# Performance work log

Measured on AMD Instinct MI355X. Metric: run time of the kernel, lower is better.

The kernel has to match this reference:

```python
import jax, jax.numpy as jnp
import numpy as np

E, H, I = 8, 2048, 768  # num_experts, hidden_size, moe_intermediate_size
B, S = 4, 1024


def setup_inputs() -> dict:
    key = jax.random.key(0)
    k1, k2, k3, k4, k5 = jax.random.split(key, 5)
    hidden_states = jax.random.normal(k1, (B, S, H), dtype=jnp.float32)
    routing_weights = jax.random.uniform(k2, (B * S, E), dtype=jnp.float32)
    router_indices = jax.random.randint(k3, (B * S, 2), 0, E)
    gate_up_proj = jax.random.normal(k4, (E, H, 2 * I), dtype=jnp.float32) * 0.02
    down_proj = jax.random.normal(k5, (E, I, H), dtype=jnp.float32) * 0.02
    return {
        "hidden_states": hidden_states,
        "routing_weights": routing_weights,
        "router_indices": router_indices,
        "gate_up_proj": gate_up_proj,
        "down_proj": down_proj,
    }


def reference(hidden_states, routing_weights, router_indices, gate_up_proj, down_proj):
    b, s, h = hidden_states.shape
    x = hidden_states.reshape(-1, h)  # [T, H], T = B*S
    # dense all-experts: every token through every expert
    gate_up = jnp.einsum("th,ehd->etd", x, gate_up_proj)  # [E, T, 2I]
    gate, up = jnp.split(gate_up, 2, axis=-1)
    inter = up * jax.nn.silu(gate)  # [E, T, I]
    out = jnp.einsum("eti,eih->eth", inter, down_proj)  # [E, T, H]
    rw = routing_weights.T.reshape(out.shape[0], b, s)  # [E, B, S]
    out = out.reshape(out.shape[0], b, s, h) * rw[..., None]
    return out.sum(axis=0)  # [B, S, H]
```

## Files before the change

### kernel.cpp

```cpp
#include <hip/hip_runtime.h>
#include <cstdint>
#include <cstddef>

#define NE 8
#define NH 2048
#define NI 768
#define NT 4096
#define NK2 6144

typedef __bf16 bf16x8 __attribute__((ext_vector_type(8)));
typedef float f32x4 __attribute__((ext_vector_type(4)));
typedef unsigned short u16x8 __attribute__((ext_vector_type(8)));

__device__ __forceinline__ unsigned short f2bf(float f) {
  unsigned int u = __builtin_bit_cast(unsigned int, f);
  u += 0x7fffu + ((u >> 16) & 1u);
  return (unsigned short)(u >> 16);
}

__device__ __forceinline__ void gload_lds16(const void* g, void* s) {
  __builtin_amdgcn_global_load_lds(
      (const __attribute__((address_space(1))) unsigned int*)g,
      (__attribute__((address_space(3))) unsigned int*)s, 16, 0, 0);
}

__global__ __launch_bounds__(256) void k_cvt(const float* __restrict__ in,
                                             unsigned short* __restrict__ out,
                                             long n) {
  long i = ((long)blockIdx.x * blockDim.x + threadIdx.x) * 8;
  if (i >= n) return;
  float4 f0 = *reinterpret_cast<const float4*>(in + i);
  float4 f1 = *reinterpret_cast<const float4*>(in + i + 4);
  u16x8 o;
  o[0] = f2bf(f0.x); o[1] = f2bf(f0.y); o[2] = f2bf(f0.z); o[3] = f2bf(f0.w);
  o[4] = f2bf(f1.x); o[5] = f2bf(f1.y); o[6] = f2bf(f1.z); o[7] = f2bf(f1.w);
  *reinterpret_cast<u16x8*>(out + i) = o;
}

__global__ __launch_bounds__(256) void k_transpose_cvt(
    const float* __restrict__ in, unsigned short* __restrict__ out,
    int R, int C, long inBS, long outBS, int outCS, int mode) {
  __shared__ float tile[32][33];
  const int b = blockIdx.z;
  const int r0 = blockIdx.y * 32, c0 = blockIdx.x * 32;
  const int tx = threadIdx.x, ty = threadIdx.y;
  const float* ib = in + (long)b * inBS;
#pragma unroll
  for (int d = 0; d < 4; d++)
    tile[ty + d * 8][tx] = ib[(long)(r0 + ty + d * 8) * C + c0 + tx];
  __syncthreads();
#pragma unroll
  for (int d = 0; d < 4; d++) {
    int c = c0 + ty + d * 8;
    int r = r0 + tx;
    int orow;
    if (mode == 1) {
      int z = (c >= NI) ? 1 : 0;
      int cc = c - z * NI;
      orow = ((cc >> 4) << 5) + (z << 4) + (cc & 15);
    } else {
      orow = c;
    }
    out[(long)b * outBS + (long)orow * outCS + r] = f2bf(tile[tx][ty + d * 8]);
  }
}


__global__ __launch_bounds__(512, 2) void k_gemm1(
    const unsigned short* __restrict__ Xb,
    const unsigned short* __restrict__ W1t,
    const float* __restrict__ rw,
    unsigned short* __restrict__ inter) {
  __shared__ unsigned short lds[2][2][16384];

  const int e = blockIdx.z;
  const int t0 = blockIdx.y * 256;
  const int bn = blockIdx.x;
  const int tid = threadIdx.x;
  const int lane = tid & 63;
  const int wave = tid >> 6;
  const int wr = wave >> 2, wc = wave & 3;
  const int fr = lane & 15, fq = lane >> 4;

  const unsigned short* Ag = Xb;
  const unsigned short* Bg = W1t + (size_t)e * (2 * NI) * NH;
  const int rowA0 = t0, rowB0 = bn * 256;
  const int nkt = NH / 64;
  const int NIT = nkt / 2;

  const int cl0 = tid, cl1 = 512 + tid;
  const int rih0 = cl0 >> 3, ck0 = cl0 & 7;
  const int rih1 = cl1 >> 3, ck1 = cl1 & 7;
  const unsigned short* sA0q0 = Ag + (size_t)(rowA0 + rih0) * NH + ((ck0 ^ (rih0 & 7)) << 3);
  const unsigned short* sA0q1 = Ag + (size_t)(rowA0 + rih1) * NH + ((ck1 ^ (rih1 & 7)) << 3);
  const unsigned short* sA1q0 = Ag + (size_t)(rowA0 + 128 + rih0) * NH + ((ck0 ^ (rih0 & 7)) << 3);
  const unsigned short* sA1q1 = Ag + (size_t)(rowA0 + 128 + rih1) * NH + ((ck1 ^ (rih1 & 7)) << 3);
  const unsigned short* sB0q0 = Bg + (size_t)(rowB0 + rih0) * NH + ((ck0 ^ (rih0 & 7)) << 3);
  const unsigned short* sB0q1 = Bg + (size_t)(rowB0 + rih1) * NH + ((ck1 ^ (rih1 & 7)) << 3);
  const unsigned short* sB1q0 = Bg + (size_t)(rowB0 + 128 + rih0) * NH + ((ck0 ^ (rih0 & 7)) << 3);
  const unsigned short* sB1q1 = Bg + (size_t)(rowB0 + 128 + rih1) * NH + ((ck1 ^ (rih1 & 7)) << 3);
  const int d0 = cl0 * 8, d1 = cl1 * 8;

#define STG_A(BUFI, H, KT) do { \
    gload_lds16(sA##H##q0 + (size_t)(KT) * 64, &lds[BUFI][0][(H) * 8192 + d0]); \
    gload_lds16(sA##H##q1 + (size_t)(KT) * 64, &lds[BUFI][0][(H) * 8192 + d1]); \
  } while (0)
#define STG_B(BUFI, H, KT) do { \
    gload_lds16(sB##H##q0 + (size_t)(KT) * 64, &lds[BUFI][1][(H) * 8192 + d0]); \
    gload_lds16(sB##H##q1 + (size_t)(KT) * 64, &lds[BUFI][1][(H) * 8192 + d1]); \
  } while (0)

  f32x4 acc[8][4];
#pragma unroll
  for (int i = 0; i < 8; ++i)
#pragma unroll
    for (int j = 0; j < 4; ++j) acc[i][j] = (f32x4){0.f, 0.f, 0.f, 0.f};

  const int swz = fr & 7;

#define PHASE(BUFI, IH, JH, ISSUE, DOWAIT) do { \
    bf16x8 af[4][2], bf[2][2]; \
    _Pragma("unroll") \
    for (int ii = 0; ii < 4; ++ii) { \
      const int rA = (IH) * 128 + wr * 64 + ii * 16 + fr; \
      _Pragma("unroll") \
      for (int kk = 0; kk < 2; ++kk) \
        af[ii][kk] = *reinterpret_cast<const bf16x8*>( \
            &lds[BUFI][0][rA * 64 + (((kk * 4 + fq) ^ swz) << 3)]); \
    } \
    _Pragma("unroll") \
    for (int jj = 0; jj < 2; ++jj) { \
      const int rB = (JH) * 128 + wc * 32 + jj * 16 + fr; \
      _Pragma("unroll") \
      for (int kk = 0; kk < 2; ++kk) \
        bf[jj][kk] = *reinterpret_cast<const bf16x8*>( \
            &lds[BUFI][1][rB * 64 + (((kk * 4 + fq) ^ swz) << 3)]); \
    } \
    ISSUE; \
    if (DOWAIT) asm volatile("s_waitcnt vmcnt(4)" ::: "memory"); \
    __builtin_amdgcn_sched_barrier(0); \
    __builtin_amdgcn_s_barrier(); \
    __builtin_amdgcn_sched_barrier(0); \
    __builtin_amdgcn_s_setprio(1); \
    _Pragma("unroll") \
    for (int kk = 0; kk < 2; ++kk) \
      _Pragma("unroll") \
      for (int ii = 0; ii < 4; ++ii) \
        _Pragma("unroll") \
        for (int jj = 0; jj < 2; ++jj) \
          acc[(IH) * 4 + ii][(JH) * 2 + jj] = __builtin_amdgcn_mfma_f32_16x16x32_bf16( \
              af[ii][kk], bf[jj][kk], acc[(IH) * 4 + ii][(JH) * 2 + jj], 0, 0, 0); \
    __builtin_amdgcn_s_setprio(0); \
    __builtin_amdgcn_sched_barrier(0); \
    __builtin_amdgcn_s_barrier(); \
    __builtin_amdgcn_sched_barrier(0); \
  } while (0)

  STG_B(0, 0, 0); STG_A(0, 0, 0); STG_A(0, 1, 0); STG_B(0, 1, 0);
  STG_B(1, 0, 1); STG_A(1, 0, 1);
  asm volatile("s_waitcnt vmcnt(4)" ::: "memory");
  __builtin_amdgcn_sched_barrier(0);
  __builtin_amdgcn_s_barrier();
  __builtin_amdgcn_sched_barrier(0);

  for (int it = 0; it < NIT; ++it) {
    const int kt1 = 2 * it + 1;
    const int p0 = (2 * it + 2 < nkt) ? 2 * it + 2 : nkt - 1;
    const int p1 = (2 * it + 3 < nkt) ? 2 * it + 3 : nkt - 1;
    PHASE(0, 0, 0, STG_A(1, 1, kt1), 0);
    PHASE(0, 1, 0, STG_B(1, 1, kt1), 0);
    PHASE(0, 0, 1, STG_B(0, 0, p0), 0);
    PHASE(0, 1, 1, STG_A(0, 0, p0), 1);
    PHASE(1, 0, 0, STG_A(0, 1, p0), 0);
    PHASE(1, 1, 0, STG_B(0, 1, p0), 0);
    PHASE(1, 0, 1, STG_B(1, 0, p1), 0);
    PHASE(1, 1, 1, STG_A(1, 0, p1), 1);
  }
  asm volatile("s_waitcnt vmcnt(0)" ::: "memory");

#undef PHASE
#undef STG_A
#undef STG_B

#pragma unroll
  for (int i = 0; i < 8; ++i) {
    const int trow = t0 + (i >> 2) * 128 + wr * 64 + (i & 3) * 16 + fq * 4;
#pragma unroll
    for (int r = 0; r < 4; ++r) {
      const int t = trow + r;
      const float rwv = rw[(size_t)t * NE + e];
#pragma unroll
      for (int p = 0; p < 2; ++p) {
        float g = acc[i][2 * p][r];
        float u = acc[i][2 * p + 1][r];
        float s = g / (1.f + __expf(-g));
        const int col = bn * 128 + (p * 4 + wc) * 16 + fr;
        inter[(size_t)t * NK2 + e * NI + col] = f2bf(rwv * u * s);
      }
    }
  }
}

#define BUF_US 24576
#define B_OFF 16384

__device__ __forceinline__ void gemm_core(
    const unsigned short* __restrict__ A, int ldA, int rowA0,
    const unsigned short* __restrict__ B, int ldB, int rowB0,
    int nkt, unsigned short* lds, f32x4 acc[4][4]) {
  const int tid = threadIdx.x;
  const int lane = tid & 63;
  const int wave = tid >> 6;
  const int wr = wave >> 1;
  const int wc = wave & 1;
  const int fr = lane & 15, fq = lane >> 4;

  size_t sA[4]; int dA[4];
#pragma unroll
  for (int q = 0; q < 4; ++q) {
    int chunk = q * 512 + tid;
    int row = chunk >> 3, c = chunk & 7;
    sA[q] = (size_t)(rowA0 + row) * ldA + ((c ^ (row & 7)) << 3);
    dA[q] = chunk * 8;
  }
  size_t sB[2]; int dB[2];
#pragma unroll
  for (int q = 0; q < 2; ++q) {
    int chunk = q * 512 + tid;
    int row = chunk >> 3, c = chunk & 7;
    sB[q] = (size_t)(rowB0 + row) * ldB + ((c ^ (row & 7)) << 3);
    dB[q] = B_OFF + chunk * 8;
  }

  int aO[2][4], bO[2][4];
#pragma unroll
  for (int kk = 0; kk < 2; ++kk) {
#pragma unroll
    for (int i = 0; i < 4; ++i) {
      int rowA = wr * 64 + i * 16 + fr;
      aO[kk][i] = rowA * 64 + (((kk * 4 + fq) ^ (rowA & 7)) << 3);
      int rowB = wc * 64 + i * 16 + fr;
      bO[kk][i] = B_OFF + rowB * 64 + (((kk * 4 + fq) ^ (rowB & 7)) << 3);
    }
  }

#pragma unroll
  for (int i = 0; i < 4; ++i)
#pragma unroll
    for (int j = 0; j < 4; ++j) acc[i][j] = (f32x4){0.f, 0.f, 0.f, 0.f};

#pragma unroll
  for (int q = 0; q < 4; ++q) gload_lds16(A + sA[q], lds + dA[q]);
#pragma unroll
  for (int q = 0; q < 2; ++q) gload_lds16(B + sB[q], lds + dB[q]);
#pragma unroll
  for (int q = 0; q < 4; ++q) gload_lds16(A + sA[q] + 64, lds + BUF_US + dA[q]);
#pragma unroll
  for (int q = 0; q < 2; ++q) gload_lds16(B + sB[q] + 64, lds + BUF_US + dB[q]);

  int bi = 0, bs = 2;
  for (int kt = 0; kt < nkt; ++kt) {
    if (kt == nkt - 1) {
      asm volatile("s_waitcnt vmcnt(0)" ::: "memory");
    } else {
      asm volatile("s_waitcnt vmcnt(6)" ::: "memory");
    }
    __builtin_amdgcn_s_barrier();
    __builtin_amdgcn_sched_barrier(0);

    if (kt + 2 < nkt) {
      const int k0 = (kt + 2) * 64;
      unsigned short* tb = lds + bs * BUF_US;
#pragma unroll
      for (int q = 0; q < 4; ++q) gload_lds16(A + sA[q] + k0, tb + dA[q]);
#pragma unroll
      for (int q = 0; q < 2; ++q) gload_lds16(B + sB[q] + k0, tb + dB[q]);
    }

    const unsigned short* cb = lds + bi * BUF_US;
#pragma unroll
    for (int kk = 0; kk < 2; ++kk) {
      bf16x8 a[4], b[4];
#pragma unroll
      for (int i = 0; i < 4; ++i) a[i] = *reinterpret_cast<const bf16x8*>(cb + aO[kk][i]);
#pragma unroll
      for (int j = 0; j < 4; ++j) b[j] = *reinterpret_cast<const bf16x8*>(cb + bO[kk][j]);
      __builtin_amdgcn_s_setprio(1);
#pragma unroll
      for (int i = 0; i < 4; ++i)
#pragma unroll
        for (int j = 0; j < 4; ++j)
          acc[i][j] = __builtin_amdgcn_mfma_f32_16x16x32_bf16(a[i], b[j], acc[i][j], 0, 0, 0);
      __builtin_amdgcn_s_setprio(0);
    }

    bi = (bi == 2) ? 0 : bi + 1;
    bs = (bs == 2) ? 0 : bs + 1;
  }
}

__global__ __launch_bounds__(512, 2) void k_gemm2(
    const unsigned short* __restrict__ inter,
    const unsigned short* __restrict__ W2t,
    float* __restrict__ out) {
  __shared__ unsigned short lds[3 * BUF_US];
  const int t0 = blockIdx.y * 256;
  const int h0 = blockIdx.x * 128;
  f32x4 acc[4][4];
  gemm_core(inter, NK2, t0, W2t, NK2, h0, NK2 / 64, lds, acc);

  const int tid = threadIdx.x, lane = tid & 63, wave = tid >> 6;
  const int wr = wave >> 1, wc = wave & 1, fr = lane & 15, fq = lane >> 4;
  const int rowBase = t0 + wr * 64 + fq * 4;
#pragma unroll
  for (int i = 0; i < 4; ++i)
#pragma unroll
    for (int j = 0; j < 4; ++j)
#pragma unroll
      for (int r = 0; r < 4; ++r)
        out[(size_t)(rowBase + i * 16 + r) * NH + h0 + wc * 64 + j * 16 + fr] =
            acc[i][j][r];
}

extern "C" void kernel_launch(void* const* d_in, const int* in_sizes, int n_in,
                              void* d_out, int out_size, void* d_ws, size_t ws_size,
                              hipStream_t stream) {
  const float* x = (const float*)d_in[0];
  const float* rw = (const float*)d_in[1];
  const float* w1 = (const float*)d_in[3];
  const float* w2 = (const float*)d_in[4];
  float* out = (float*)d_out;

  char* ws = (char*)d_ws;
  unsigned short* Xb = (unsigned short*)ws;
  unsigned short* W1t = (unsigned short*)(ws + 16777216);
  unsigned short* W2t = (unsigned short*)(ws + 16777216 + 50331648);
  unsigned short* inter = (unsigned short*)(ws + 16777216 + 50331648 + 25165824);

  k_cvt<<<dim3((NT * NH) / (256 * 8)), dim3(256), 0, stream>>>(x, Xb, (long)NT * NH);
  k_transpose_cvt<<<dim3((2 * NI) / 32, NH / 32, NE), dim3(32, 8), 0, stream>>>(
      w1, W1t, NH, 2 * NI, (long)NH * 2 * NI, (long)2 * NI * NH, NH, 1);
  k_transpose_cvt<<<dim3(NH / 32, NI / 32, NE), dim3(32, 8), 0, stream>>>(
      w2, W2t, NI, NH, (long)NI * NH, (long)NI, NK2, 0);
  k_gemm1<<<dim3((2 * NI) / 256, NT / 256, NE), dim3(512), 0, stream>>>(Xb, W1t, rw, inter);
  k_gemm2<<<dim3(NH / 128, NT / 256), dim3(512), 0, stream>>>(inter, W2t, out);
}
```

Measured before the change: 372.2 us.

## Reuse B fragments across paired phases and drop trailing per-phase barrier

B-operand fragments are now loaded from LDS only on alternate phases and kept in registers for the next phase, which halves B LDS reads. The second workgroup barrier at the end of each phase is removed, leaving one barrier per phase. The order of the global-to-LDS staging calls is rearranged so that each buffer region is refilled only after every wave has passed the barrier following its last read. This cuts synchronization and LDS traffic, but it raises register pressure and depends on the new issue order being correct to avoid read/write races.

```diff
diff --git a/kernel.cpp b/kernel.cpp
--- a/kernel.cpp
+++ b/kernel.cpp
@@ -117,9 +117,20 @@
     for (int j = 0; j < 4; ++j) acc[i][j] = (f32x4){0.f, 0.f, 0.f, 0.f};
 
   const int swz = fr & 7;
-
-#define PHASE(BUFI, IH, JH, ISSUE, DOWAIT) do { \
-    bf16x8 af[4][2], bf[2][2]; \
+  bf16x8 bfr[2][2];
+
+#define PHASE(BUFI, IH, JH, RDB, ISSUE, DOWAIT) do { \
+    if (RDB) { \
+      _Pragma("unroll") \
+      for (int jj = 0; jj < 2; ++jj) { \
+        const int rB = (JH) * 128 + wc * 32 + jj * 16 + fr; \
+        _Pragma("unroll") \
+        for (int kk = 0; kk < 2; ++kk) \
+          bfr[jj][kk] = *reinterpret_cast<const bf16x8*>( \
+              &lds[BUFI][1][rB * 64 + (((kk * 4 + fq) ^ swz) << 3)]); \
+      } \
+    } \
+    bf16x8 af[4][2]; \
     _Pragma("unroll") \
     for (int ii = 0; ii < 4; ++ii) { \
       const int rA = (IH) * 128 + wr * 64 + ii * 16 + fr; \
@@ -127,14 +138,6 @@
       for (int kk = 0; kk < 2; ++kk) \
         af[ii][kk] = *reinterpret_cast<const bf16x8*>( \
             &lds[BUFI][0][rA * 64 + (((kk * 4 + fq) ^ swz) << 3)]); \
-    } \
-    _Pragma("unroll") \
-    for (int jj = 0; jj < 2; ++jj) { \
-      const int rB = (JH) * 128 + wc * 32 + jj * 16 + fr; \
-      _Pragma("unroll") \
-      for (int kk = 0; kk < 2; ++kk) \
-        bf[jj][kk] = *reinterpret_cast<const bf16x8*>( \
-            &lds[BUFI][1][rB * 64 + (((kk * 4 + fq) ^ swz) << 3)]); \
     } \
     ISSUE; \
     if (DOWAIT) asm volatile("s_waitcnt vmcnt(4)" ::: "memory"); \
@@ -149,10 +152,8 @@
         _Pragma("unroll") \
         for (int jj = 0; jj < 2; ++jj) \
           acc[(IH) * 4 + ii][(JH) * 2 + jj] = __builtin_amdgcn_mfma_f32_16x16x32_bf16( \
-              af[ii][kk], bf[jj][kk], acc[(IH) * 4 + ii][(JH) * 2 + jj], 0, 0, 0); \
+              af[ii][kk], bfr[jj][kk], acc[(IH) * 4 + ii][(JH) * 2 + jj], 0, 0, 0); \
     __builtin_amdgcn_s_setprio(0); \
-    __builtin_amdgcn_sched_barrier(0); \
-    __builtin_amdgcn_s_barrier(); \
     __builtin_amdgcn_sched_barrier(0); \
   } while (0)
 
@@ -165,16 +166,16 @@
 
   for (int it = 0; it < NIT; ++it) {
     const int kt1 = 2 * it + 1;
-    const int p0 = (2 * it + 2 < nkt) ? 2 * it + 2 : nkt - 1;
-    const int p1 = (2 * it + 3 < nkt) ? 2 * it + 3 : nkt - 1;
-    PHASE(0, 0, 0, STG_A(1, 1, kt1), 0);
-    PHASE(0, 1, 0, STG_B(1, 1, kt1), 0);
-    PHASE(0, 0, 1, STG_B(0, 0, p0), 0);
-    PHASE(0, 1, 1, STG_A(0, 0, p0), 1);
-    PHASE(1, 0, 0, STG_A(0, 1, p0), 0);
-    PHASE(1, 1, 0, STG_B(0, 1, p0), 0);
-    PHASE(1, 0, 1, STG_B(1, 0, p1), 0);
-    PHASE(1, 1, 1, STG_A(1, 0, p1), 1);
+    const int kt2 = (2 * it + 2 < nkt) ? 2 * it + 2 : nkt - 1;
+    const int kt3 = (2 * it + 3 < nkt) ? 2 * it + 3 : nkt - 1;
+    PHASE(0, 0, 0, 1, STG_B(1, 1, kt1), 0);
+    PHASE(0, 1, 0, 0, STG_A(1, 1, kt1), 0);
+    PHASE(0, 0, 1, 1, STG_B(0, 0, kt2), 0);
+    PHASE(0, 1, 1, 0, STG_A(0, 0, kt2), 1);
+    PHASE(1, 0, 0, 1, STG_B(0, 1, kt2), 0);
+    PHASE(1, 1, 0, 0, STG_A(0, 1, kt2), 0);
+    PHASE(1, 0, 1, 1, STG_B(1, 0, kt3), 0);
+    PHASE(1, 1, 1, 0, STG_A(1, 0, kt3), 1);
   }
   asm volatile("s_waitcnt vmcnt(0)" ::: "memory");
 
```

Result: faster. 349.8 us (-6.0%).
